# Performance work log

Hardware: AMD Instinct MI355X
Metric: run time of the kernel (lower is better)

## Reference

```python
import jax, jax.numpy as jnp
from jax import lax
import numpy as np

T, B, I, H = 365, 2048, 9, 50


def setup_inputs() -> dict:
    key = jax.random.key(0)
    ks = jax.random.split(key, 12)
    s = 0.1
    return {
        "x": jax.random.normal(ks[0], (T, B, I), dtype=jnp.float32),
        "w_ih0": jax.random.normal(ks[1], (4 * H, I), dtype=jnp.float32) * s,
        "w_hh0": jax.random.normal(ks[2], (4 * H, H), dtype=jnp.float32) * s,
        "b_ih0": jax.random.normal(ks[3], (4 * H,), dtype=jnp.float32) * s,
        "b_hh0": jax.random.normal(ks[4], (4 * H,), dtype=jnp.float32) * s,
        "w_ih1": jax.random.normal(ks[5], (4 * H, H), dtype=jnp.float32) * s,
        "w_hh1": jax.random.normal(ks[6], (4 * H, H), dtype=jnp.float32) * s,
        "b_ih1": jax.random.normal(ks[7], (4 * H,), dtype=jnp.float32) * s,
        "b_hh1": jax.random.normal(ks[8], (4 * H,), dtype=jnp.float32) * s,
        "fc_w": jax.random.normal(ks[9], (1, H), dtype=jnp.float32) * s,
        "fc_b": jax.random.normal(ks[10], (1,), dtype=jnp.float32) * s,
    }


def _lstm_layer(x, w_ih, w_hh, b_ih, b_hh):
    # x: [T, B, in]; PyTorch gate order: i, f, g, o
    Bq = x.shape[1]
    Hh = w_hh.shape[1]
    # precompute input projections for all timesteps (one big GEMM)
    x_proj = jnp.einsum('tbi,gi->tbg', x, w_ih) + b_ih + b_hh  # [T, B, 4H]

    def step(carry, xp):
        h, c = carry
        gates = xp + h @ w_hh.T  # [B, 4H]
        i, f, g, o = jnp.split(gates, 4, axis=-1)
        i = jax.nn.sigmoid(i)
        f = jax.nn.sigmoid(f)
        g = jnp.tanh(g)
        o = jax.nn.sigmoid(o)
        c = f * c + i * g
        h = o * jnp.tanh(c)
        return (h, c), h

    h0 = jnp.zeros((Bq, Hh), dtype=x.dtype)
    _, hs = lax.scan(step, (h0, h0), x_proj)
    return hs  # [T, B, H]


def reference(x, w_ih0, w_hh0, b_ih0, b_hh0, w_ih1, w_hh1, b_ih1, b_hh1, fc_w, fc_b):
    h1 = _lstm_layer(x, w_ih0, w_hh0, b_ih0, b_hh0)
    h2 = _lstm_layer(h1, w_ih1, w_hh1, b_ih1, b_hh1)
    out = jnp.einsum('tbh,oh->tbo', h2, fc_w) + fc_b  # [T, B, 1]
    return out
```

## Files before the change

kernel.cpp:

```cpp
#include <hip/hip_runtime.h>

#define T_STEPS 365
#define BATCH   2048
#define INP     9
#define HID     50
#define G4      200
#define MB      16
#define NBLK    (BATCH/MB)
#define NT      512
#define NW      8
#define NTILES  13
#define TPW     2

typedef __attribute__((ext_vector_type(8))) short short8;
typedef __attribute__((ext_vector_type(4))) float float4v;

__device__ __forceinline__ unsigned short f2bf(float v) {
    unsigned u = __builtin_bit_cast(unsigned, v);
    unsigned r = (u + 0x7FFFu + ((u >> 16) & 1u)) >> 16;
    return (unsigned short)r;
}
__device__ __forceinline__ float sig_(float x) {
    return __builtin_amdgcn_rcpf(1.f + __expf(-x));
}
__device__ __forceinline__ float tanh_(float x) {
    return 1.f - 2.f * __builtin_amdgcn_rcpf(__expf(2.f * x) + 1.f);
}

__device__ __forceinline__ int hx_off(int m, int k) {
    return (m * 128 + k) ^ ((m & 7) << 3);
}

__global__ __launch_bounds__(NT, 1)
void lstm_mfma(const float* __restrict__ x,
               const float* __restrict__ w_ih0, const float* __restrict__ w_hh0,
               const float* __restrict__ b_ih0, const float* __restrict__ b_hh0,
               const float* __restrict__ w_ih1, const float* __restrict__ w_hh1,
               const float* __restrict__ b_ih1, const float* __restrict__ b_hh1,
               const float* __restrict__ fc_w, const float* __restrict__ fc_b,
               float* __restrict__ out)
{
    __shared__ __align__(16) unsigned short HX[2][MB * 128];
    __shared__ float FCP[NW][MB];

    const int t   = threadIdx.x;
    const int w   = t >> 6;
    const int lid = t & 63;
    const int mcol = lid & 15;
    const int kgrp = lid >> 4;
    const int kb8  = kgrp * 8;
    const int b0   = blockIdx.x * MB;
    const float fcb = fc_b[0];

    short8 wA0[TPW][2];
    short8 wA1[TPW][4];
    float  bs0[TPW][4], bs1[TPW][4], fcw[TPW];
    float  c0s[TPW], c1s[TPW];

    #pragma unroll
    for (int tt = 0; tt < TPW; ++tt) {
        const int T  = tt * 8 + w;
        const bool tv = (T < NTILES);
        const int r  = T * 16 + mcol;
        const bool rv = tv && (r < G4);
        const int u  = r >> 2, g = r & 3;
        const int orig = g * HID + u;
        #pragma unroll
        for (int kt = 0; kt < 2; ++kt) {
            short8 f;
            #pragma unroll
            for (int j = 0; j < 8; ++j) {
                int k = kt * 32 + kb8 + j;
                float v = 0.f;
                if (rv) {
                    if (k < HID)            v = w_hh0[orig * HID + k];
                    else if (k < HID + INP) v = w_ih0[orig * INP + (k - HID)];
                }
                f[j] = (short)f2bf(v);
            }
            wA0[tt][kt] = f;
        }
        #pragma unroll
        for (int kt = 0; kt < 4; ++kt) {
            short8 f;
            #pragma unroll
            for (int j = 0; j < 8; ++j) {
                int k = kt * 32 + kb8 + j;
                float v = 0.f;
                if (rv) {
                    if (k < HID)                      v = w_ih1[orig * HID + k];
                    else if (k >= 64 && k < 64 + HID) v = w_hh1[orig * HID + (k - 64)];
                }
                f[j] = (short)f2bf(v);
            }
            wA1[tt][kt] = f;
        }
        const int u_lane = T * 4 + kgrp;
        #pragma unroll
        for (int rr = 0; rr < 4; ++rr) {
            int row = T * 16 + kgrp * 4 + rr;
            bool bv = tv && (row < G4);
            int uu = row >> 2, gg = row & 3;
            bs0[tt][rr] = bv ? (b_ih0[gg * HID + uu] + b_hh0[gg * HID + uu]) : 0.f;
            bs1[tt][rr] = bv ? (b_ih1[gg * HID + uu] + b_hh1[gg * HID + uu]) : 0.f;
        }
        fcw[tt] = (tv && u_lane < HID) ? fc_w[u_lane] : 0.f;
        c0s[tt] = 0.f; c1s[tt] = 0.f;
    }

    for (int i = t; i < 2 * MB * 128; i += NT) (&HX[0][0])[i] = 0;
    if (t < NW * MB) (&FCP[0][0])[t] = 0.f;
    __syncthreads();
    const bool xth = (t < MB * INP);
    const int  xm = t / INP, xj = t - xm * INP;
    if (xth) HX[0][hx_off(xm, HID + xj)] = f2bf(x[(size_t)(b0 + xm) * INP + xj]);
    __syncthreads();

    for (int step = 0; step < T_STEPS; ++step) {
        const int cur = step & 1, nxt = cur ^ 1;

        float xv = 0.f;
        const int sp1 = step + 1;
        if (xth && sp1 < T_STEPS)
            xv = x[((size_t)sp1 * BATCH + b0 + xm) * INP + xj];

        short8 hx0 = *(const short8*)&HX[cur][hx_off(mcol, kb8)];
        short8 hx1 = *(const short8*)&HX[cur][hx_off(mcol, 32 + kb8)];
        float h0v[TPW];
        #pragma unroll
        for (int tt = 0; tt < TPW; ++tt) {
            float4v acc = {bs0[tt][0], bs0[tt][1], bs0[tt][2], bs0[tt][3]};
            acc = __builtin_amdgcn_mfma_f32_16x16x32_bf16(wA0[tt][0], hx0, acc, 0, 0, 0);
            acc = __builtin_amdgcn_mfma_f32_16x16x32_bf16(wA0[tt][1], hx1, acc, 0, 0, 0);
            float gi = sig_(acc[0]), gf = sig_(acc[1]);
            float gg = tanh_(acc[2]), go = sig_(acc[3]);
            c0s[tt] = gf * c0s[tt] + gi * gg;
            h0v[tt] = go * tanh_(c0s[tt]);
        }
        #pragma unroll
        for (int tt = 0; tt < TPW; ++tt) {
            int T = tt * 8 + w, u = T * 4 + kgrp;
            if (T < NTILES && u < HID)
                HX[nxt][hx_off(mcol, u)] = f2bf(h0v[tt]);
        }
        if (xth && sp1 < T_STEPS)
            HX[nxt][hx_off(xm, HID + xj)] = f2bf(xv);
        __syncthreads();

        short8 a0 = *(const short8*)&HX[nxt][hx_off(mcol, kb8)];
        short8 a1 = *(const short8*)&HX[nxt][hx_off(mcol, 32 + kb8)];
        short8 a2 = *(const short8*)&HX[cur][hx_off(mcol, 64 + kb8)];
        short8 a3 = *(const short8*)&HX[cur][hx_off(mcol, 96 + kb8)];
        float fcp = 0.f;
        float h1v[TPW];
        #pragma unroll
        for (int tt = 0; tt < TPW; ++tt) {
            float4v acc = {bs1[tt][0], bs1[tt][1], bs1[tt][2], bs1[tt][3]};
            acc = __builtin_amdgcn_mfma_f32_16x16x32_bf16(wA1[tt][0], a0, acc, 0, 0, 0);
            acc = __builtin_amdgcn_mfma_f32_16x16x32_bf16(wA1[tt][1], a1, acc, 0, 0, 0);
            acc = __builtin_amdgcn_mfma_f32_16x16x32_bf16(wA1[tt][2], a2, acc, 0, 0, 0);
            acc = __builtin_amdgcn_mfma_f32_16x16x32_bf16(wA1[tt][3], a3, acc, 0, 0, 0);
            float gi = sig_(acc[0]), gf = sig_(acc[1]);
            float gg = tanh_(acc[2]), go = sig_(acc[3]);
            c1s[tt] = gf * c1s[tt] + gi * gg;
            h1v[tt] = go * tanh_(c1s[tt]);
            fcp += fcw[tt] * h1v[tt];
        }
        fcp += __shfl_xor(fcp, 16);
        fcp += __shfl_xor(fcp, 32);
        if (lid < MB) FCP[w][lid] = fcp;
        #pragma unroll
        for (int tt = 0; tt < TPW; ++tt) {
            int T = tt * 8 + w, u = T * 4 + kgrp;
            if (T < NTILES && u < HID)
                HX[nxt][hx_off(mcol, 64 + u)] = f2bf(h1v[tt]);
        }
        __syncthreads();

        if (t < MB) {
            float s = fcb;
            #pragma unroll
            for (int ww = 0; ww < NW; ++ww) s += FCP[ww][t];
            out[(size_t)step * BATCH + b0 + t] = s;
        }
    }
}

extern "C" void kernel_launch(void* const* d_in, const int* in_sizes, int n_in,
                              void* d_out, int out_size, void* d_ws, size_t ws_size,
                              hipStream_t stream) {
    const float* x     = (const float*)d_in[0];
    const float* w_ih0 = (const float*)d_in[1];
    const float* w_hh0 = (const float*)d_in[2];
    const float* b_ih0 = (const float*)d_in[3];
    const float* b_hh0 = (const float*)d_in[4];
    const float* w_ih1 = (const float*)d_in[5];
    const float* w_hh1 = (const float*)d_in[6];
    const float* b_ih1 = (const float*)d_in[7];
    const float* b_hh1 = (const float*)d_in[8];
    const float* fc_w  = (const float*)d_in[9];
    const float* fc_b  = (const float*)d_in[10];
    float* out = (float*)d_out;

    lstm_mfma<<<dim3(NBLK), dim3(NT), 0, stream>>>(
        x, w_ih0, w_hh0, b_ih0, b_hh0,
        w_ih1, w_hh1, b_ih1, b_hh1, fc_w, fc_b, out);
}
```

Measured before the change: 382.5 us.

## Wavefront-pipeline the two LSTM layers across warp groups with one barrier per phase

Warps are split into two groups: four warps run layer 0 for step t while the other four run layer 1 for step t-1. This halves the barriers per timestep from two to one and lets the two layers' MFMA and activation work overlap. The x prefetch and the output reduction move onto the layer-0 warps, with the write delayed by two phases. Each warp now holds up to four tiles of weights, which raises register pressure. Launch bounds are relaxed to allow two blocks per CU, but the layer-0 group is now serialised over four tiles per warp instead of two.

```diff
diff --git a/kernel.cpp b/kernel.cpp
--- a/kernel.cpp
+++ b/kernel.cpp
@@ -4,13 +4,10 @@
 #define BATCH   2048
 #define INP     9
 #define HID     50
-#define G4      200
 #define MB      16
 #define NBLK    (BATCH/MB)
 #define NT      512
-#define NW      8
 #define NTILES  13
-#define TPW     2
 
 typedef __attribute__((ext_vector_type(8))) short short8;
 typedef __attribute__((ext_vector_type(4))) float float4v;
@@ -31,8 +28,8 @@
     return (m * 128 + k) ^ ((m & 7) << 3);
 }
 
-__global__ __launch_bounds__(NT, 1)
-void lstm_mfma(const float* __restrict__ x,
+__global__ __launch_bounds__(NT, 2)
+void lstm_pipe(const float* __restrict__ x,
                const float* __restrict__ w_ih0, const float* __restrict__ w_hh0,
                const float* __restrict__ b_ih0, const float* __restrict__ b_hh0,
                const float* __restrict__ w_ih1, const float* __restrict__ w_hh1,
@@ -41,148 +38,168 @@
                float* __restrict__ out)
 {
     __shared__ __align__(16) unsigned short HX[2][MB * 128];
-    __shared__ float FCP[NW][MB];
-
-    const int t   = threadIdx.x;
-    const int w   = t >> 6;
-    const int lid = t & 63;
+    __shared__ float FCP[2][4][MB];
+
+    const int t    = threadIdx.x;
+    const int w    = t >> 6;
+    const int lid  = t & 63;
     const int mcol = lid & 15;
     const int kgrp = lid >> 4;
     const int kb8  = kgrp * 8;
     const int b0   = blockIdx.x * MB;
+    const bool isL1 = (w < 4);
+    const int v    = isL1 ? w : (w - 4);
     const float fcb = fc_b[0];
 
-    short8 wA0[TPW][2];
-    short8 wA1[TPW][4];
-    float  bs0[TPW][4], bs1[TPW][4], fcw[TPW];
-    float  c0s[TPW], c1s[TPW];
+    short8 wA[4][4];
+    float  bs[4][4], fcw[4], cst[4];
+    const float* bih = isL1 ? b_ih1 : b_ih0;
+    const float* bhh = isL1 ? b_hh1 : b_hh0;
 
     #pragma unroll
-    for (int tt = 0; tt < TPW; ++tt) {
-        const int T  = tt * 8 + w;
+    for (int tt = 0; tt < 4; ++tt) {
+        const int T  = v + 4 * tt;
         const bool tv = (T < NTILES);
         const int r  = T * 16 + mcol;
-        const bool rv = tv && (r < G4);
-        const int u  = r >> 2, g = r & 3;
-        const int orig = g * HID + u;
-        #pragma unroll
-        for (int kt = 0; kt < 2; ++kt) {
-            short8 f;
+        const bool rv = tv && (r < 4 * HID);
+        const int u_r = r >> 2, g_r = r & 3;
+        const int orig = g_r * HID + u_r;
+        if (isL1) {
             #pragma unroll
-            for (int j = 0; j < 8; ++j) {
-                int k = kt * 32 + kb8 + j;
-                float v = 0.f;
-                if (rv) {
-                    if (k < HID)            v = w_hh0[orig * HID + k];
-                    else if (k < HID + INP) v = w_ih0[orig * INP + (k - HID)];
-                }
-                f[j] = (short)f2bf(v);
-            }
-            wA0[tt][kt] = f;
-        }
-        #pragma unroll
-        for (int kt = 0; kt < 4; ++kt) {
-            short8 f;
+            for (int kt = 0; kt < 4; ++kt) {
+                short8 f;
+                #pragma unroll
+                for (int j = 0; j < 8; ++j) {
+                    int k = kt * 32 + kb8 + j;
+                    float val = 0.f;
+                    if (rv) {
+                        if (k < HID)                      val = w_ih1[orig * HID + k];
+                        else if (k >= 64 && k < 64 + HID) val = w_hh1[orig * HID + (k - 64)];
+                    }
+                    f[j] = (short)f2bf(val);
+                }
+                wA[tt][kt] = f;
+            }
+        } else {
             #pragma unroll
-            for (int j = 0; j < 8; ++j) {
-                int k = kt * 32 + kb8 + j;
-                float v = 0.f;
-                if (rv) {
-                    if (k < HID)                      v = w_ih1[orig * HID + k];
-                    else if (k >= 64 && k < 64 + HID) v = w_hh1[orig * HID + (k - 64)];
-                }
-                f[j] = (short)f2bf(v);
-            }
-            wA1[tt][kt] = f;
+            for (int kt = 0; kt < 2; ++kt) {
+                short8 f;
+                #pragma unroll
+                for (int j = 0; j < 8; ++j) {
+                    int k = kt * 32 + kb8 + j;
+                    float val = 0.f;
+                    if (rv) {
+                        if (k < HID)            val = w_hh0[orig * HID + k];
+                        else if (k < HID + INP) val = w_ih0[orig * INP + (k - HID)];
+                    }
+                    f[j] = (short)f2bf(val);
+                }
+                wA[tt][kt] = f;
+            }
+            wA[tt][2] = short8{}; wA[tt][3] = short8{};
         }
         const int u_lane = T * 4 + kgrp;
         #pragma unroll
         for (int rr = 0; rr < 4; ++rr) {
             int row = T * 16 + kgrp * 4 + rr;
-            bool bv = tv && (row < G4);
-            int uu = row >> 2, gg = row & 3;
-            bs0[tt][rr] = bv ? (b_ih0[gg * HID + uu] + b_hh0[gg * HID + uu]) : 0.f;
-            bs1[tt][rr] = bv ? (b_ih1[gg * HID + uu] + b_hh1[gg * HID + uu]) : 0.f;
+            bool bvv = tv && (row < 4 * HID);
+            int uu = row >> 2;
+            bs[tt][rr] = bvv ? (bih[rr * HID + uu] + bhh[rr * HID + uu]) : 0.f;
         }
-        fcw[tt] = (tv && u_lane < HID) ? fc_w[u_lane] : 0.f;
-        c0s[tt] = 0.f; c1s[tt] = 0.f;
+        fcw[tt] = (isL1 && tv && u_lane < HID) ? fc_w[u_lane] : 0.f;
+        cst[tt] = 0.f;
     }
 
+    int xi = -1;
+    if (w == 4) xi = lid;
+    else if (w == 5) xi = 64 + lid;
+    else if (w == 6 && lid < 16) xi = 128 + lid;
+    const bool xact = (xi >= 0 && xi < MB * INP);
+    const int xm = xact ? xi / INP : 0, xj = xact ? xi % INP : 0;
+
     for (int i = t; i < 2 * MB * 128; i += NT) (&HX[0][0])[i] = 0;
-    if (t < NW * MB) (&FCP[0][0])[t] = 0.f;
+    if (t < 2 * 4 * MB) (&FCP[0][0][0])[t] = 0.f;
     __syncthreads();
-    const bool xth = (t < MB * INP);
-    const int  xm = t / INP, xj = t - xm * INP;
-    if (xth) HX[0][hx_off(xm, HID + xj)] = f2bf(x[(size_t)(b0 + xm) * INP + xj]);
+    float xreg = 0.f;
+    if (xact) {
+        HX[1][hx_off(xm, HID + xj)] = f2bf(x[(size_t)(b0 + xm) * INP + xj]);
+        xreg = x[((size_t)BATCH + b0 + xm) * INP + xj];
+    }
     __syncthreads();
 
-    for (int step = 0; step < T_STEPS; ++step) {
-        const int cur = step & 1, nxt = cur ^ 1;
-
-        float xv = 0.f;
-        const int sp1 = step + 1;
-        if (xth && sp1 < T_STEPS)
-            xv = x[((size_t)sp1 * BATCH + b0 + xm) * INP + xj];
-
-        short8 hx0 = *(const short8*)&HX[cur][hx_off(mcol, kb8)];
-        short8 hx1 = *(const short8*)&HX[cur][hx_off(mcol, 32 + kb8)];
-        float h0v[TPW];
-        #pragma unroll
-        for (int tt = 0; tt < TPW; ++tt) {
-            float4v acc = {bs0[tt][0], bs0[tt][1], bs0[tt][2], bs0[tt][3]};
-            acc = __builtin_amdgcn_mfma_f32_16x16x32_bf16(wA0[tt][0], hx0, acc, 0, 0, 0);
-            acc = __builtin_amdgcn_mfma_f32_16x16x32_bf16(wA0[tt][1], hx1, acc, 0, 0, 0);
-            float gi = sig_(acc[0]), gf = sig_(acc[1]);
-            float gg = tanh_(acc[2]), go = sig_(acc[3]);
-            c0s[tt] = gf * c0s[tt] + gi * gg;
-            h0v[tt] = go * tanh_(c0s[tt]);
-        }
-        #pragma unroll
-        for (int tt = 0; tt < TPW; ++tt) {
-            int T = tt * 8 + w, u = T * 4 + kgrp;
-            if (T < NTILES && u < HID)
-                HX[nxt][hx_off(mcol, u)] = f2bf(h0v[tt]);
-        }
-        if (xth && sp1 < T_STEPS)
-            HX[nxt][hx_off(xm, HID + xj)] = f2bf(xv);
-        __syncthreads();
-
-        short8 a0 = *(const short8*)&HX[nxt][hx_off(mcol, kb8)];
-        short8 a1 = *(const short8*)&HX[nxt][hx_off(mcol, 32 + kb8)];
-        short8 a2 = *(const short8*)&HX[cur][hx_off(mcol, 64 + kb8)];
-        short8 a3 = *(const short8*)&HX[cur][hx_off(mcol, 96 + kb8)];
-        float fcp = 0.f;
-        float h1v[TPW];
-        #pragma unroll
-        for (int tt = 0; tt < TPW; ++tt) {
-            float4v acc = {bs1[tt][0], bs1[tt][1], bs1[tt][2], bs1[tt][3]};
-            acc = __builtin_amdgcn_mfma_f32_16x16x32_bf16(wA1[tt][0], a0, acc, 0, 0, 0);
-            acc = __builtin_amdgcn_mfma_f32_16x16x32_bf16(wA1[tt][1], a1, acc, 0, 0, 0);
-            acc = __builtin_amdgcn_mfma_f32_16x16x32_bf16(wA1[tt][2], a2, acc, 0, 0, 0);
-            acc = __builtin_amdgcn_mfma_f32_16x16x32_bf16(wA1[tt][3], a3, acc, 0, 0, 0);
-            float gi = sig_(acc[0]), gf = sig_(acc[1]);
-            float gg = tanh_(acc[2]), go = sig_(acc[3]);
-            c1s[tt] = gf * c1s[tt] + gi * gg;
-            h1v[tt] = go * tanh_(c1s[tt]);
-            fcp += fcw[tt] * h1v[tt];
-        }
-        fcp += __shfl_xor(fcp, 16);
-        fcp += __shfl_xor(fcp, 32);
-        if (lid < MB) FCP[w][lid] = fcp;
-        #pragma unroll
-        for (int tt = 0; tt < TPW; ++tt) {
-            int T = tt * 8 + w, u = T * 4 + kgrp;
-            if (T < NTILES && u < HID)
-                HX[nxt][hx_off(mcol, 64 + u)] = f2bf(h1v[tt]);
+    for (int ph = 0; ph < T_STEPS + 2; ++ph) {
+        const int cur = (ph + 1) & 1, nxt = ph & 1;
+
+        short8 f0 = *(const short8*)&HX[cur][hx_off(mcol, kb8)];
+        short8 f1 = *(const short8*)&HX[cur][hx_off(mcol, 32 + kb8)];
+
+        if (isL1) {
+            if (ph >= 1 && ph <= T_STEPS) {
+                short8 f2 = *(const short8*)&HX[cur][hx_off(mcol, 64 + kb8)];
+                short8 f3 = *(const short8*)&HX[cur][hx_off(mcol, 96 + kb8)];
+                float h1v[4];
+                float fcp = 0.f;
+                #pragma unroll
+                for (int tt = 0; tt < 4; ++tt) {
+                    const int T = v + 4 * tt;
+                    if (T < NTILES) {
+                        float4v acc = {bs[tt][0], bs[tt][1], bs[tt][2], bs[tt][3]};
+                        acc = __builtin_amdgcn_mfma_f32_16x16x32_bf16(wA[tt][0], f0, acc, 0, 0, 0);
+                        acc = __builtin_amdgcn_mfma_f32_16x16x32_bf16(wA[tt][1], f1, acc, 0, 0, 0);
+                        acc = __builtin_amdgcn_mfma_f32_16x16x32_bf16(wA[tt][2], f2, acc, 0, 0, 0);
+                        acc = __builtin_amdgcn_mfma_f32_16x16x32_bf16(wA[tt][3], f3, acc, 0, 0, 0);
+                        float gi = sig_(acc[0]), gf = sig_(acc[1]);
+                        float gg = tanh_(acc[2]), go = sig_(acc[3]);
+                        cst[tt] = gf * cst[tt] + gi * gg;
+                        h1v[tt] = go * tanh_(cst[tt]);
+                        fcp += fcw[tt] * h1v[tt];
+                    }
+                }
+                #pragma unroll
+                for (int tt = 0; tt < 4; ++tt) {
+                    const int T = v + 4 * tt, u = T * 4 + kgrp;
+                    if (T < NTILES && u < HID)
+                        HX[nxt][hx_off(mcol, 64 + u)] = f2bf(h1v[tt]);
+                }
+                fcp += __shfl_xor(fcp, 16);
+                fcp += __shfl_xor(fcp, 32);
+                if (lid < MB) FCP[ph & 1][v][lid] = fcp;
+            }
+        } else {
+            if (ph < T_STEPS) {
+                float h0v[4];
+                #pragma unroll
+                for (int tt = 0; tt < 4; ++tt) {
+                    const int T = v + 4 * tt;
+                    if (T < NTILES) {
+                        float4v acc = {bs[tt][0], bs[tt][1], bs[tt][2], bs[tt][3]};
+                        acc = __builtin_amdgcn_mfma_f32_16x16x32_bf16(wA[tt][0], f0, acc, 0, 0, 0);
+                        acc = __builtin_amdgcn_mfma_f32_16x16x32_bf16(wA[tt][1], f1, acc, 0, 0, 0);
+                        float gi = sig_(acc[0]), gf = sig_(acc[1]);
+                        float gg = tanh_(acc[2]), go = sig_(acc[3]);
+                        cst[tt] = gf * cst[tt] + gi * gg;
+                        h0v[tt] = go * tanh_(cst[tt]);
+                    }
+                }
+                #pragma unroll
+                for (int tt = 0; tt < 4; ++tt) {
+                    const int T = v + 4 * tt, u = T * 4 + kgrp;
+                    if (T < NTILES && u < HID)
+                        HX[nxt][hx_off(mcol, u)] = f2bf(h0v[tt]);
+                }
+            }
+            if (xact) {
+                if (ph + 1 < T_STEPS) HX[nxt][hx_off(xm, HID + xj)] = f2bf(xreg);
+                if (ph + 2 < T_STEPS) xreg = x[((size_t)(ph + 2) * BATCH + b0 + xm) * INP + xj];
+            }
+            if (w == 7 && lid < MB && ph >= 2) {
+                const int rp = (ph - 1) & 1;
+                float s = fcb + FCP[rp][0][lid] + FCP[rp][1][lid]
+                              + FCP[rp][2][lid] + FCP[rp][3][lid];
+                out[(size_t)(ph - 2) * BATCH + b0 + lid] = s;
+            }
         }
         __syncthreads();
-
-        if (t < MB) {
-            float s = fcb;
-            #pragma unroll
-            for (int ww = 0; ww < NW; ++ww) s += FCP[ww][t];
-            out[(size_t)step * BATCH + b0 + t] = s;
-        }
     }
 }
 
@@ -202,7 +219,7 @@
     const float* fc_b  = (const float*)d_in[10];
     float* out = (float*)d_out;
 
-    lstm_mfma<<<dim3(NBLK), dim3(NT), 0, stream>>>(
+    lstm_pipe<<<dim3(NBLK), dim3(NT), 0, stream>>>(
         x, w_ih0, w_hh0, b_ih0, b_hh0,
         w_ih1, w_hh1, b_ih1, b_hh1, fc_w, fc_b, out);
 }
```

Result: faster. 369.8 us (-3.3%).
